# Performance work log

Measured on AMD Instinct MI355X. Metric: run time of the kernel, lower is better.

Reference implementation:

```python
import jax, jax.numpy as jnp
import numpy as np

N_NODES = 50000
N_EDGES = 1600000
IN_SIZE = 128
HIDDEN = 128
OUT_SIZE = 64
NUM_LAYERS = 3
BN_EPS = 1e-5
GIN_EPS_INIT = 1e-5


def setup_inputs() -> dict:
    key = jax.random.key(0)
    ks = jax.random.split(key, 16)
    node_feat = jax.random.normal(ks[0], (N_NODES, IN_SIZE), dtype=jnp.float32)
    src = jax.random.randint(ks[1], (N_EDGES,), 0, N_NODES)
    dst = jax.random.randint(ks[2], (N_EDGES,), 0, N_NODES)
    # per-layer MLP params (in_size == hidden, so shapes are uniform across layers)
    s1 = 1.0 / np.sqrt(IN_SIZE)
    s2 = 1.0 / np.sqrt(HIDDEN)
    W1 = jax.random.uniform(ks[3], (NUM_LAYERS, IN_SIZE, HIDDEN), jnp.float32, -s1, s1)
    b1 = jax.random.uniform(ks[4], (NUM_LAYERS, HIDDEN), jnp.float32, -s1, s1)
    gamma = jnp.ones((NUM_LAYERS, HIDDEN), jnp.float32)
    beta = jnp.zeros((NUM_LAYERS, HIDDEN), jnp.float32)
    W2 = jax.random.uniform(ks[5], (NUM_LAYERS, HIDDEN, HIDDEN), jnp.float32, -s2, s2)
    b2 = jax.random.uniform(ks[6], (NUM_LAYERS, HIDDEN), jnp.float32, -s2, s2)
    eps = jnp.full((NUM_LAYERS,), GIN_EPS_INIT, jnp.float32)  # learnable GIN eps
    Wout = jax.random.uniform(ks[7], (HIDDEN, OUT_SIZE), jnp.float32, -s2, s2)
    bout = jax.random.uniform(ks[8], (OUT_SIZE,), jnp.float32, -s2, s2)
    return {"node_feat": node_feat, "src": src, "dst": dst,
            "W1": W1, "b1": b1, "gamma": gamma, "beta": beta,
            "W2": W2, "b2": b2, "eps": eps, "Wout": Wout, "bout": bout}


def reference(node_feat, src, dst, W1, b1, gamma, beta, W2, b2, eps, Wout, bout):
    n = node_feat.shape[0]
    h = node_feat
    for i in range(NUM_LAYERS):
        # sum-aggregate source features onto destination nodes
        agg = jax.ops.segment_sum(h[src], dst, num_segments=n)  # [N, d]
        x = (1.0 + eps[i]) * h + agg
        x = x @ W1[i] + b1[i]
        # BatchNorm1d (training mode: batch statistics, biased variance)
        mu = jnp.mean(x, axis=0)
        var = jnp.var(x, axis=0)
        x = (x - mu) * jax.lax.rsqrt(var + BN_EPS) * gamma[i] + beta[i]
        x = jax.nn.relu(x)
        h = jax.nn.relu(x @ W2[i] + b2[i])
    return h @ Wout + bout
```

## Files before the change

kernel.cpp:

```cpp
#include <hip/hip_runtime.h>

#define NN 50000
#define NE 1600000
#define HID 128
#define NB 196
#define BCAP 12288

typedef _Float16 half8 __attribute__((ext_vector_type(8)));
typedef float floatx4 __attribute__((ext_vector_type(4)));


__global__ __launch_bounds__(256) void kb_count(const int* __restrict__ dst,
                                                int* __restrict__ gcnt, int E) {
  __shared__ int cnt[NB];
  int tid = threadIdx.x;
  for (int i = tid; i < NB; i += 256) cnt[i] = 0;
  __syncthreads();
  int base = blockIdx.x * 4096;
  for (int i = 0; i < 16; ++i) {
    int e = base + i * 256 + tid;
    if (e < E) atomicAdd(&cnt[dst[e] >> 8], 1);
  }
  __syncthreads();
  for (int i = tid; i < NB; i += 256)
    if (cnt[i]) atomicAdd(&gcnt[i], cnt[i]);
}

__global__ __launch_bounds__(256) void kb_basescan(const int* __restrict__ gcnt,
                                                   int* __restrict__ bbase,
                                                   int* __restrict__ bcur) {
  __shared__ int s[256];
  int tid = threadIdx.x;
  int v = (tid < NB) ? gcnt[tid] : 0;
  s[tid] = v;
  __syncthreads();
  for (int d = 1; d < 256; d <<= 1) {
    int t = (tid >= d) ? s[tid - d] : 0;
    __syncthreads();
    s[tid] += t;
    __syncthreads();
  }
  int incl = s[tid];
  if (tid < NB) {
    bbase[tid] = incl - v;
    bcur[tid] = incl - v;
  }
  if (tid == NB - 1) bbase[NB] = incl;
}

__global__ __launch_bounds__(256) void kb_partition(const int* __restrict__ src,
                                                    const int* __restrict__ dst,
                                                    int* __restrict__ bcur,
                                                    int2* __restrict__ ebuf, int E) {
  __shared__ int cnt[NB];
  __shared__ int sbase[NB];
  int tid = threadIdx.x;
  for (int i = tid; i < NB; i += 256) cnt[i] = 0;
  __syncthreads();
  int base = blockIdx.x * 4096;
  int myd[16], mys[16];
#pragma unroll
  for (int i = 0; i < 16; ++i) {
    int e = base + i * 256 + tid;
    if (e < E) {
      myd[i] = dst[e];
      mys[i] = src[e];
      atomicAdd(&cnt[myd[i] >> 8], 1);
    } else {
      myd[i] = -1;
    }
  }
  __syncthreads();
  for (int i = tid; i < NB; i += 256)
    sbase[i] = cnt[i] ? atomicAdd(&bcur[i], cnt[i]) : 0;
  __syncthreads();
  for (int i = tid; i < NB; i += 256) cnt[i] = 0;
  __syncthreads();
#pragma unroll
  for (int i = 0; i < 16; ++i) {
    if (myd[i] >= 0) {
      int b = myd[i] >> 8;
      int r = atomicAdd(&cnt[b], 1);
      ebuf[sbase[b] + r] = make_int2(mys[i], myd[i]);
    }
  }
}

__global__ __launch_bounds__(256) void kb_csr(const int2* __restrict__ ebuf,
                                              const int* __restrict__ bbase,
                                              int* __restrict__ rs,
                                              int* __restrict__ eidx, int M) {
  __shared__ int cnt[256];
  __shared__ int off[256];
  __shared__ int sbuf[BCAP];
  int tid = threadIdx.x;
  int b = blockIdx.x;
  int lo = bbase[b], hi = bbase[b + 1];
  int n = hi - lo;
  cnt[tid] = 0;
  __syncthreads();
  for (int i = tid; i < n; i += 256) atomicAdd(&cnt[ebuf[lo + i].y & 255], 1);
  __syncthreads();
  int v = cnt[tid];
  off[tid] = v;
  __syncthreads();
  for (int d = 1; d < 256; d <<= 1) {
    int t = (tid >= d) ? off[tid - d] : 0;
    __syncthreads();
    off[tid] += t;
    __syncthreads();
  }
  int excl = off[tid] - v;
  int gnode = b * 256 + tid;
  if (gnode < M) rs[gnode] = lo + excl;
  if (b == NB - 1 && tid == 0) rs[M] = bbase[NB];
  __syncthreads();
  cnt[tid] = excl;
  __syncthreads();
  if (n <= BCAP) {
    for (int i = tid; i < n; i += 256) {
      int2 ed = ebuf[lo + i];
      int r = atomicAdd(&cnt[ed.y & 255], 1);
      sbuf[r] = ed.x;
    }
    __syncthreads();
    for (int i = tid; i < n; i += 256) eidx[lo + i] = sbuf[i];
  } else {
    for (int i = tid; i < n; i += 256) {
      int2 ed = ebuf[lo + i];
      int r = atomicAdd(&cnt[ed.y & 255], 1);
      eidx[lo + r] = ed.x;
    }
  }
}


__global__ __launch_bounds__(256) void k_cvt(const float* __restrict__ x,
                                             _Float16* __restrict__ y, int n8) {
  int t = blockIdx.x * 256 + threadIdx.x;
  if (t >= n8) return;
  const float4* x4 = (const float4*)x;
  float4 u = x4[t * 2], v = x4[t * 2 + 1];
  half8 o;
  o[0] = (_Float16)u.x; o[1] = (_Float16)u.y; o[2] = (_Float16)u.z; o[3] = (_Float16)u.w;
  o[4] = (_Float16)v.x; o[5] = (_Float16)v.y; o[6] = (_Float16)v.z; o[7] = (_Float16)v.w;
  ((half8*)y)[t] = o;
}


__global__ __launch_bounds__(256) void k_pack(const float* __restrict__ W1,
                                              const float* __restrict__ W2,
                                              const float* __restrict__ Wout,
                                              _Float16* __restrict__ wp) {
  int y = blockIdx.y;
  const float* W;
  _Float16* dst;
  int NCT;
  if (y < 3) { W = W1 + (size_t)y * 16384; dst = wp + y * 16384; NCT = 8; }
  else if (y < 6) { W = W2 + (size_t)(y - 3) * 16384; dst = wp + 49152 + (y - 3) * 16384; NCT = 8; }
  else { W = Wout; dst = wp + 98304; NCT = 4; }
  int t = blockIdx.x * 256 + threadIdx.x;
  if (t >= 4 * NCT * 64) return;
  int lane = t & 63;
  int ct = (t >> 6) % NCT;
  int kb = t / (64 * NCT);
  int n = ct * 16 + (lane & 15);
  int k0 = kb * 32 + (lane >> 4) * 8;
  int N = NCT * 16;
#pragma unroll
  for (int j = 0; j < 8; ++j) dst[t * 8 + j] = (_Float16)W[(k0 + j) * N + n];
}


__global__ __launch_bounds__(1024, 8) void k_aggemm1(
    const int* __restrict__ rs, const int* __restrict__ eidx,
    const float* __restrict__ eps, int layer, const _Float16* __restrict__ h,
    const _Float16* __restrict__ wp1, const float* __restrict__ b1L,
    float* __restrict__ csum, float* __restrict__ csq,
    _Float16* __restrict__ x) {
  __shared__ _Float16 As[64 * 136];
  __shared__ float sredS[512];
  __shared__ float sredQ[512];
  const int tid = threadIdx.x;
  const int wid = tid >> 6;
  const int lane = tid & 63;
  const int slot = lane >> 4;
  const int c8 = lane & 15;
  const int rowBase = blockIdx.x * 64;
  const float ep = 1.0f + eps[layer];
  const half8* h8 = (const half8*)h;

  for (int i = 0; i < 4; ++i) {
    const int node = rowBase + wid * 4 + i;
    float a0[8] = {0, 0, 0, 0, 0, 0, 0, 0};
    float a1[8] = {0, 0, 0, 0, 0, 0, 0, 0};
    float a2[8] = {0, 0, 0, 0, 0, 0, 0, 0};
    float a3[8] = {0, 0, 0, 0, 0, 0, 0, 0};
    int e0 = 0, e1 = 0;
    if (node < NN) {
      e0 = rs[node];
      e1 = rs[node + 1];
    }
    int e = e0 + slot;
    for (; e + 12 < e1; e += 16) {
      int s0 = eidx[e];
      int s1 = eidx[e + 4];
      int s2 = eidx[e + 8];
      int s3 = eidx[e + 12];
      half8 v0 = h8[s0 * 16 + c8];
      half8 v1 = h8[s1 * 16 + c8];
      half8 v2 = h8[s2 * 16 + c8];
      half8 v3 = h8[s3 * 16 + c8];
#pragma unroll
      for (int j = 0; j < 8; ++j) {
        a0[j] += (float)v0[j];
        a1[j] += (float)v1[j];
        a2[j] += (float)v2[j];
        a3[j] += (float)v3[j];
      }
    }
    for (; e < e1; e += 4) {
      half8 v = h8[eidx[e] * 16 + c8];
#pragma unroll
      for (int j = 0; j < 8; ++j) a0[j] += (float)v[j];
    }
#pragma unroll
    for (int j = 0; j < 8; ++j) {
      a0[j] += a1[j] + a2[j] + a3[j];
      a0[j] += __shfl_xor(a0[j], 16);
      a0[j] += __shfl_xor(a0[j], 32);
    }
    if (slot == 0) {
      half8 o = {0, 0, 0, 0, 0, 0, 0, 0};
      if (node < NN) {
        half8 hv = h8[node * 16 + c8];
#pragma unroll
        for (int j = 0; j < 8; ++j) o[j] = (_Float16)fmaf(ep, (float)hv[j], a0[j]);
      }
      *(half8*)(As + (wid * 4 + i) * 136 + c8 * 8) = o;
    }
  }
  __syncthreads();

  const int rg = wid & 3;
  const int cg = wid >> 2;
  floatx4 acc[2];
  acc[0] = (floatx4){0.f, 0.f, 0.f, 0.f};
  acc[1] = (floatx4){0.f, 0.f, 0.f, 0.f};
  const half8* wp8 = (const half8*)wp1;
#pragma unroll
  for (int kb = 0; kb < 4; ++kb) {
    half8 a = *(const half8*)(As + (rg * 16 + c8) * 136 + kb * 32 + slot * 8);
#pragma unroll
    for (int t = 0; t < 2; ++t) {
      int ct = cg * 2 + t;
      acc[t] = __builtin_amdgcn_mfma_f32_16x16x32_f16(a, wp8[(kb * 8 + ct) * 64 + lane],
                                                      acc[t], 0, 0, 0);
    }
  }
#pragma unroll
  for (int t = 0; t < 2; ++t) {
    int ct = cg * 2 + t;
    float bv = b1L[ct * 16 + c8];
    float ps = 0.f, pq = 0.f;
#pragma unroll
    for (int reg = 0; reg < 4; ++reg) {
      int row = rg * 16 + slot * 4 + reg;
      int gr = rowBase + row;
      float xv = acc[t][reg] + bv;
      if (gr < NN) {
        x[(size_t)gr * 128 + ct * 16 + c8] = (_Float16)xv;
        ps += xv;
        pq += xv * xv;
      }
    }
    ps += __shfl_xor(ps, 16);
    ps += __shfl_xor(ps, 32);
    pq += __shfl_xor(pq, 16);
    pq += __shfl_xor(pq, 32);
    if (lane < 16) {
      sredS[wid * 32 + t * 16 + lane] = ps;
      sredQ[wid * 32 + t * 16 + lane] = pq;
    }
  }
  __syncthreads();
  if (tid < 128) {
    int c = tid;
    int wbase = (c >> 5) * 4;
    int loc = c & 31;
    float s = sredS[wbase * 32 + loc] + sredS[(wbase + 1) * 32 + loc] +
              sredS[(wbase + 2) * 32 + loc] + sredS[(wbase + 3) * 32 + loc];
    atomicAdd(&csum[c], s);
  } else if (tid < 256) {
    int c = tid - 128;
    int wbase = (c >> 5) * 4;
    int loc = c & 31;
    float q = sredQ[wbase * 32 + loc] + sredQ[(wbase + 1) * 32 + loc] +
              sredQ[(wbase + 2) * 32 + loc] + sredQ[(wbase + 3) * 32 + loc];
    atomicAdd(&csq[c], q);
  }
}


template <int FINAL>
__global__ __launch_bounds__(1024, 8) void k_bn_gemm2(
    const _Float16* __restrict__ x, const _Float16* __restrict__ wp2,
    const float* __restrict__ b2L, const float* __restrict__ gammaL,
    const float* __restrict__ betaL, const float* __restrict__ csum,
    const float* __restrict__ csq, _Float16* __restrict__ hout,
    const _Float16* __restrict__ wpo, const float* __restrict__ boutp,
    float* __restrict__ out) {
  __shared__ _Float16 As[64 * 136];
  const int tid = threadIdx.x;
  const int wid = tid >> 6;
  const int lane = tid & 63;
  const int slot = lane >> 4;
  const int c8 = lane & 15;
  const int c8t = tid & 15;
  const int rowBase = blockIdx.x * 64;

  float sc[8], sh[8];
  {
    const float invM = 1.0f / (float)NN;
#pragma unroll
    for (int j = 0; j < 8; ++j) {
      int k = c8t * 8 + j;
      float mu = csum[k] * invM;
      float var = csq[k] * invM - mu * mu;
      float g = gammaL[k] * rsqrtf(var + 1e-5f);
      sc[j] = g;
      sh[j] = fmaf(-mu, g, betaL[k]);
    }
  }
  {
    int row = tid >> 4;
    int gr = rowBase + row;
    half8 v = {0, 0, 0, 0, 0, 0, 0, 0};
    if (gr < NN) {
      v = *(const half8*)(x + (size_t)gr * 128 + c8t * 8);
#pragma unroll
      for (int j = 0; j < 8; ++j)
        v[j] = (_Float16)fmaxf(fmaf((float)v[j], sc[j], sh[j]), 0.f);
    }
    *(half8*)(As + row * 136 + c8t * 8) = v;
  }
  __syncthreads();

  const int rg = wid & 3;
  const int cg = wid >> 2;
  floatx4 acc[2];
  acc[0] = (floatx4){0.f, 0.f, 0.f, 0.f};
  acc[1] = (floatx4){0.f, 0.f, 0.f, 0.f};
  const half8* wp8 = (const half8*)wp2;
#pragma unroll
  for (int kb = 0; kb < 4; ++kb) {
    half8 a = *(const half8*)(As + (rg * 16 + c8) * 136 + kb * 32 + slot * 8);
#pragma unroll
    for (int t = 0; t < 2; ++t) {
      int ct = cg * 2 + t;
      acc[t] = __builtin_amdgcn_mfma_f32_16x16x32_f16(a, wp8[(kb * 8 + ct) * 64 + lane],
                                                      acc[t], 0, 0, 0);
    }
  }
  __syncthreads();
#pragma unroll
  for (int t = 0; t < 2; ++t) {
    int ct = cg * 2 + t;
    float bv = b2L[ct * 16 + c8];
#pragma unroll
    for (int reg = 0; reg < 4; ++reg) {
      int row = rg * 16 + slot * 4 + reg;
      As[row * 136 + ct * 16 + c8] = (_Float16)fmaxf(acc[t][reg] + bv, 0.f);
    }
  }
  __syncthreads();

  if (FINAL == 0) {
    int row = tid >> 4;
    int gr = rowBase + row;
    if (gr < NN) {
      half8 v = *(half8*)(As + row * 136 + c8t * 8);
      *(half8*)(hout + (size_t)gr * 128 + c8t * 8) = v;
    }
  } else {
    if (cg < 2) {
      floatx4 acc3[2];
      acc3[0] = (floatx4){0.f, 0.f, 0.f, 0.f};
      acc3[1] = (floatx4){0.f, 0.f, 0.f, 0.f};
      const half8* wo8 = (const half8*)wpo;
#pragma unroll
      for (int kb = 0; kb < 4; ++kb) {
        half8 a = *(const half8*)(As + (rg * 16 + c8) * 136 + kb * 32 + slot * 8);
#pragma unroll
        for (int t = 0; t < 2; ++t) {
          int ct = cg * 2 + t;
          acc3[t] = __builtin_amdgcn_mfma_f32_16x16x32_f16(
              a, wo8[(kb * 4 + ct) * 64 + lane], acc3[t], 0, 0, 0);
        }
      }
#pragma unroll
      for (int t = 0; t < 2; ++t) {
        int ct = cg * 2 + t;
        float bv = boutp[ct * 16 + c8];
#pragma unroll
        for (int reg = 0; reg < 4; ++reg) {
          int gr = rowBase + rg * 16 + slot * 4 + reg;
          if (gr < NN) out[(size_t)gr * 64 + ct * 16 + c8] = acc3[t][reg] + bv;
        }
      }
    }
  }
}


extern "C" void kernel_launch(void* const* d_in, const int* in_sizes, int n_in,
                              void* d_out, int out_size, void* d_ws, size_t ws_size,
                              hipStream_t stream) {
  const float* node_feat = (const float*)d_in[0];
  const int* src = (const int*)d_in[1];
  const int* dst = (const int*)d_in[2];
  const float* W1 = (const float*)d_in[3];
  const float* b1 = (const float*)d_in[4];
  const float* gamma = (const float*)d_in[5];
  const float* beta = (const float*)d_in[6];
  const float* W2 = (const float*)d_in[7];
  const float* b2 = (const float*)d_in[8];
  const float* eps = (const float*)d_in[9];
  const float* Wout = (const float*)d_in[10];
  const float* bout = (const float*)d_in[11];
  float* out = (float*)d_out;

  int* rs = (int*)d_ws;
  int* gcnt = rs + 50176;
  int* bbase = gcnt + 256;
  int* bcur = bbase + 256;
  float* stats = (float*)(bcur + 256);
  int* eidx = (int*)(stats + 768);
  _Float16* hb = (_Float16*)(eidx + NE);
  _Float16* xb = hb + (size_t)NN * HID;
  _Float16* wp = xb + (size_t)NN * HID;
  int2* ebuf = (int2*)(wp + 106496);

  hipMemsetAsync(gcnt, 0, (256 * 3 + 768) * sizeof(int), stream);

  k_cvt<<<(NN * HID / 8 + 255) / 256, 256, 0, stream>>>(node_feat, hb, NN * HID / 8);
  k_pack<<<dim3(8, 7), 256, 0, stream>>>(W1, W2, Wout, wp);

  const int partGrid = (NE + 4095) / 4096;
  kb_count<<<partGrid, 256, 0, stream>>>(dst, gcnt, NE);
  kb_basescan<<<1, 256, 0, stream>>>(gcnt, bbase, bcur);
  kb_partition<<<partGrid, 256, 0, stream>>>(src, dst, bcur, ebuf, NE);
  kb_csr<<<NB, 256, 0, stream>>>(ebuf, bbase, rs, eidx, NN);

  const int rowTiles = (NN + 63) / 64;

  for (int L = 0; L < 3; ++L) {
    float* csum = stats + L * 256;
    float* csq = csum + 128;
    k_aggemm1<<<rowTiles, 1024, 0, stream>>>(
        rs, eidx, eps, L, hb, wp + (size_t)L * 16384, b1 + (size_t)L * HID,
        csum, csq, xb);
    if (L < 2) {
      k_bn_gemm2<0><<<rowTiles, 1024, 0, stream>>>(
          xb, wp + 49152 + (size_t)L * 16384, b2 + (size_t)L * HID,
          gamma + (size_t)L * HID, beta + (size_t)L * HID, csum, csq, hb,
          nullptr, nullptr, nullptr);
    } else {
      k_bn_gemm2<1><<<rowTiles, 1024, 0, stream>>>(
          xb, wp + 49152 + (size_t)L * 16384, b2 + (size_t)L * HID,
          gamma + (size_t)L * HID, beta + (size_t)L * HID, csum, csq, nullptr,
          wp + 98304, bout, out);
    }
  }
}
```

Measured before the change: 450.7 us.

## Use persistent blocks with atomic tile counter for aggregate and GEMM kernels

Both the aggregation+GEMM1 kernel and the BN+GEMM2 kernel now launch a fixed grid of 512 persistent 1024-thread blocks. Each block repeatedly grabs 64-row tiles from a global atomic counter, and one counter per launch is zeroed by the existing memset. This is meant to even out load imbalance from irregular node degrees and to amortize per-block setup such as BN scale/shift. The aggregation kernel also stages its GEMM1 output in shared memory so it can write coalesced half8 rows. The cost is extra barriers and an atomic per tile, and the larger per-block count may limit occupancy.

```diff
diff --git a/kernel.cpp b/kernel.cpp
--- a/kernel.cpp
+++ b/kernel.cpp
@@ -5,6 +5,8 @@
 #define HID 128
 #define NB 196
 #define BCAP 12288
+#define NTILES 782
+#define PBLK 512
 
 typedef _Float16 half8 __attribute__((ext_vector_type(8)));
 typedef float floatx4 __attribute__((ext_vector_type(4)));
@@ -177,127 +179,146 @@
     const float* __restrict__ eps, int layer, const _Float16* __restrict__ h,
     const _Float16* __restrict__ wp1, const float* __restrict__ b1L,
     float* __restrict__ csum, float* __restrict__ csq,
-    _Float16* __restrict__ x) {
+    _Float16* __restrict__ x, int* __restrict__ tctr) {
   __shared__ _Float16 As[64 * 136];
   __shared__ float sredS[512];
   __shared__ float sredQ[512];
+  __shared__ int stile;
   const int tid = threadIdx.x;
   const int wid = tid >> 6;
   const int lane = tid & 63;
   const int slot = lane >> 4;
   const int c8 = lane & 15;
-  const int rowBase = blockIdx.x * 64;
+  const int c8t = tid & 15;
   const float ep = 1.0f + eps[layer];
   const half8* h8 = (const half8*)h;
-
-  for (int i = 0; i < 4; ++i) {
-    const int node = rowBase + wid * 4 + i;
-    float a0[8] = {0, 0, 0, 0, 0, 0, 0, 0};
-    float a1[8] = {0, 0, 0, 0, 0, 0, 0, 0};
-    float a2[8] = {0, 0, 0, 0, 0, 0, 0, 0};
-    float a3[8] = {0, 0, 0, 0, 0, 0, 0, 0};
-    int e0 = 0, e1 = 0;
-    if (node < NN) {
-      e0 = rs[node];
-      e1 = rs[node + 1];
-    }
-    int e = e0 + slot;
-    for (; e + 12 < e1; e += 16) {
-      int s0 = eidx[e];
-      int s1 = eidx[e + 4];
-      int s2 = eidx[e + 8];
-      int s3 = eidx[e + 12];
-      half8 v0 = h8[s0 * 16 + c8];
-      half8 v1 = h8[s1 * 16 + c8];
-      half8 v2 = h8[s2 * 16 + c8];
-      half8 v3 = h8[s3 * 16 + c8];
-#pragma unroll
-      for (int j = 0; j < 8; ++j) {
-        a0[j] += (float)v0[j];
-        a1[j] += (float)v1[j];
-        a2[j] += (float)v2[j];
-        a3[j] += (float)v3[j];
-      }
-    }
-    for (; e < e1; e += 4) {
-      half8 v = h8[eidx[e] * 16 + c8];
-#pragma unroll
-      for (int j = 0; j < 8; ++j) a0[j] += (float)v[j];
-    }
-#pragma unroll
-    for (int j = 0; j < 8; ++j) {
-      a0[j] += a1[j] + a2[j] + a3[j];
-      a0[j] += __shfl_xor(a0[j], 16);
-      a0[j] += __shfl_xor(a0[j], 32);
-    }
-    if (slot == 0) {
-      half8 o = {0, 0, 0, 0, 0, 0, 0, 0};
-      if (node < NN) {
-        half8 hv = h8[node * 16 + c8];
-#pragma unroll
-        for (int j = 0; j < 8; ++j) o[j] = (_Float16)fmaf(ep, (float)hv[j], a0[j]);
-      }
-      *(half8*)(As + (wid * 4 + i) * 136 + c8 * 8) = o;
-    }
-  }
-  __syncthreads();
-
+  const half8* wp8 = (const half8*)wp1;
   const int rg = wid & 3;
   const int cg = wid >> 2;
-  floatx4 acc[2];
-  acc[0] = (floatx4){0.f, 0.f, 0.f, 0.f};
-  acc[1] = (floatx4){0.f, 0.f, 0.f, 0.f};
-  const half8* wp8 = (const half8*)wp1;
-#pragma unroll
-  for (int kb = 0; kb < 4; ++kb) {
-    half8 a = *(const half8*)(As + (rg * 16 + c8) * 136 + kb * 32 + slot * 8);
+
+  while (true) {
+    if (tid == 0) stile = atomicAdd(tctr, 1);
+    __syncthreads();
+    const int tile = stile;
+    if (tile >= NTILES) break;
+    const int rowBase = tile * 64;
+
+    for (int i = 0; i < 4; ++i) {
+      const int node = rowBase + wid * 4 + i;
+      float a0[8] = {0, 0, 0, 0, 0, 0, 0, 0};
+      float a1[8] = {0, 0, 0, 0, 0, 0, 0, 0};
+      float a2[8] = {0, 0, 0, 0, 0, 0, 0, 0};
+      float a3[8] = {0, 0, 0, 0, 0, 0, 0, 0};
+      int e0 = 0, e1 = 0;
+      if (node < NN) {
+        e0 = rs[node];
+        e1 = rs[node + 1];
+      }
+      int e = e0 + slot;
+      for (; e + 12 < e1; e += 16) {
+        int s0 = eidx[e];
+        int s1 = eidx[e + 4];
+        int s2 = eidx[e + 8];
+        int s3 = eidx[e + 12];
+        half8 v0 = h8[s0 * 16 + c8];
+        half8 v1 = h8[s1 * 16 + c8];
+        half8 v2 = h8[s2 * 16 + c8];
+        half8 v3 = h8[s3 * 16 + c8];
+#pragma unroll
+        for (int j = 0; j < 8; ++j) {
+          a0[j] += (float)v0[j];
+          a1[j] += (float)v1[j];
+          a2[j] += (float)v2[j];
+          a3[j] += (float)v3[j];
+        }
+      }
+      for (; e < e1; e += 4) {
+        half8 v = h8[eidx[e] * 16 + c8];
+#pragma unroll
+        for (int j = 0; j < 8; ++j) a0[j] += (float)v[j];
+      }
+#pragma unroll
+      for (int j = 0; j < 8; ++j) {
+        a0[j] += a1[j] + a2[j] + a3[j];
+        a0[j] += __shfl_xor(a0[j], 16);
+        a0[j] += __shfl_xor(a0[j], 32);
+      }
+      if (slot == 0) {
+        half8 o = {0, 0, 0, 0, 0, 0, 0, 0};
+        if (node < NN) {
+          half8 hv = h8[node * 16 + c8];
+#pragma unroll
+          for (int j = 0; j < 8; ++j) o[j] = (_Float16)fmaf(ep, (float)hv[j], a0[j]);
+        }
+        *(half8*)(As + (wid * 4 + i) * 136 + c8 * 8) = o;
+      }
+    }
+    __syncthreads();
+
+    floatx4 acc[2];
+    acc[0] = (floatx4){0.f, 0.f, 0.f, 0.f};
+    acc[1] = (floatx4){0.f, 0.f, 0.f, 0.f};
+#pragma unroll
+    for (int kb = 0; kb < 4; ++kb) {
+      half8 a = *(const half8*)(As + (rg * 16 + c8) * 136 + kb * 32 + slot * 8);
+#pragma unroll
+      for (int t = 0; t < 2; ++t) {
+        int ct = cg * 2 + t;
+        acc[t] = __builtin_amdgcn_mfma_f32_16x16x32_f16(
+            a, wp8[(kb * 8 + ct) * 64 + lane], acc[t], 0, 0, 0);
+      }
+    }
+    __syncthreads();
+
 #pragma unroll
     for (int t = 0; t < 2; ++t) {
       int ct = cg * 2 + t;
-      acc[t] = __builtin_amdgcn_mfma_f32_16x16x32_f16(a, wp8[(kb * 8 + ct) * 64 + lane],
-                                                      acc[t], 0, 0, 0);
-    }
-  }
-#pragma unroll
-  for (int t = 0; t < 2; ++t) {
-    int ct = cg * 2 + t;
-    float bv = b1L[ct * 16 + c8];
-    float ps = 0.f, pq = 0.f;
-#pragma unroll
-    for (int reg = 0; reg < 4; ++reg) {
-      int row = rg * 16 + slot * 4 + reg;
+      float bv = b1L[ct * 16 + c8];
+      float ps = 0.f, pq = 0.f;
+#pragma unroll
+      for (int reg = 0; reg < 4; ++reg) {
+        int row = rg * 16 + slot * 4 + reg;
+        float xv = acc[t][reg] + bv;
+        As[row * 136 + ct * 16 + c8] = (_Float16)xv;
+        if (rowBase + row < NN) {
+          ps += xv;
+          pq += xv * xv;
+        }
+      }
+      ps += __shfl_xor(ps, 16);
+      ps += __shfl_xor(ps, 32);
+      pq += __shfl_xor(pq, 16);
+      pq += __shfl_xor(pq, 32);
+      if (lane < 16) {
+        sredS[wid * 32 + t * 16 + lane] = ps;
+        sredQ[wid * 32 + t * 16 + lane] = pq;
+      }
+    }
+    __syncthreads();
+
+    {
+      int row = tid >> 4;
       int gr = rowBase + row;
-      float xv = acc[t][reg] + bv;
       if (gr < NN) {
-        x[(size_t)gr * 128 + ct * 16 + c8] = (_Float16)xv;
-        ps += xv;
-        pq += xv * xv;
-      }
-    }
-    ps += __shfl_xor(ps, 16);
-    ps += __shfl_xor(ps, 32);
-    pq += __shfl_xor(pq, 16);
-    pq += __shfl_xor(pq, 32);
-    if (lane < 16) {
-      sredS[wid * 32 + t * 16 + lane] = ps;
-      sredQ[wid * 32 + t * 16 + lane] = pq;
-    }
-  }
-  __syncthreads();
-  if (tid < 128) {
-    int c = tid;
-    int wbase = (c >> 5) * 4;
-    int loc = c & 31;
-    float s = sredS[wbase * 32 + loc] + sredS[(wbase + 1) * 32 + loc] +
-              sredS[(wbase + 2) * 32 + loc] + sredS[(wbase + 3) * 32 + loc];
-    atomicAdd(&csum[c], s);
-  } else if (tid < 256) {
-    int c = tid - 128;
-    int wbase = (c >> 5) * 4;
-    int loc = c & 31;
-    float q = sredQ[wbase * 32 + loc] + sredQ[(wbase + 1) * 32 + loc] +
-              sredQ[(wbase + 2) * 32 + loc] + sredQ[(wbase + 3) * 32 + loc];
-    atomicAdd(&csq[c], q);
+        half8 v = *(half8*)(As + row * 136 + c8t * 8);
+        *(half8*)(x + (size_t)gr * 128 + c8t * 8) = v;
+      }
+    }
+    if (tid < 128) {
+      int c = tid;
+      int wbase = (c >> 5) * 4;
+      int loc = c & 31;
+      float s = sredS[wbase * 32 + loc] + sredS[(wbase + 1) * 32 + loc] +
+                sredS[(wbase + 2) * 32 + loc] + sredS[(wbase + 3) * 32 + loc];
+      atomicAdd(&csum[c], s);
+    } else if (tid < 256) {
+      int c = tid - 128;
+      int wbase = (c >> 5) * 4;
+      int loc = c & 31;
+      float q = sredQ[wbase * 32 + loc] + sredQ[(wbase + 1) * 32 + loc] +
+                sredQ[(wbase + 2) * 32 + loc] + sredQ[(wbase + 3) * 32 + loc];
+      atomicAdd(&csq[c], q);
+    }
   }
 }
 
@@ -309,15 +330,17 @@
     const float* __restrict__ betaL, const float* __restrict__ csum,
     const float* __restrict__ csq, _Float16* __restrict__ hout,
     const _Float16* __restrict__ wpo, const float* __restrict__ boutp,
-    float* __restrict__ out) {
+    float* __restrict__ out, int* __restrict__ tctr) {
   __shared__ _Float16 As[64 * 136];
+  __shared__ int stile;
   const int tid = threadIdx.x;
   const int wid = tid >> 6;
   const int lane = tid & 63;
   const int slot = lane >> 4;
   const int c8 = lane & 15;
   const int c8t = tid & 15;
-  const int rowBase = blockIdx.x * 64;
+  const int rg = wid & 3;
+  const int cg = wid >> 2;
 
   float sc[8], sh[8];
   {
@@ -332,82 +355,90 @@
       sh[j] = fmaf(-mu, g, betaL[k]);
     }
   }
-  {
-    int row = tid >> 4;
-    int gr = rowBase + row;
-    half8 v = {0, 0, 0, 0, 0, 0, 0, 0};
-    if (gr < NN) {
-      v = *(const half8*)(x + (size_t)gr * 128 + c8t * 8);
-#pragma unroll
-      for (int j = 0; j < 8; ++j)
-        v[j] = (_Float16)fmaxf(fmaf((float)v[j], sc[j], sh[j]), 0.f);
-    }
-    *(half8*)(As + row * 136 + c8t * 8) = v;
-  }
-  __syncthreads();
-
-  const int rg = wid & 3;
-  const int cg = wid >> 2;
-  floatx4 acc[2];
-  acc[0] = (floatx4){0.f, 0.f, 0.f, 0.f};
-  acc[1] = (floatx4){0.f, 0.f, 0.f, 0.f};
-  const half8* wp8 = (const half8*)wp2;
-#pragma unroll
-  for (int kb = 0; kb < 4; ++kb) {
-    half8 a = *(const half8*)(As + (rg * 16 + c8) * 136 + kb * 32 + slot * 8);
+
+  while (true) {
+    if (tid == 0) stile = atomicAdd(tctr, 1);
+    __syncthreads();
+    const int tile = stile;
+    if (tile >= NTILES) break;
+    const int rowBase = tile * 64;
+
+    {
+      int row = tid >> 4;
+      int gr = rowBase + row;
+      half8 v = {0, 0, 0, 0, 0, 0, 0, 0};
+      if (gr < NN) {
+        v = *(const half8*)(x + (size_t)gr * 128 + c8t * 8);
+#pragma unroll
+        for (int j = 0; j < 8; ++j)
+          v[j] = (_Float16)fmaxf(fmaf((float)v[j], sc[j], sh[j]), 0.f);
+      }
+      *(half8*)(As + row * 136 + c8t * 8) = v;
+    }
+    __syncthreads();
+
+    floatx4 acc[2];
+    acc[0] = (floatx4){0.f, 0.f, 0.f, 0.f};
+    acc[1] = (floatx4){0.f, 0.f, 0.f, 0.f};
+    const half8* wp8 = (const half8*)wp2;
+#pragma unroll
+    for (int kb = 0; kb < 4; ++kb) {
+      half8 a = *(const half8*)(As + (rg * 16 + c8) * 136 + kb * 32 + slot * 8);
+#pragma unroll
+      for (int t = 0; t < 2; ++t) {
+        int ct = cg * 2 + t;
+        acc[t] = __builtin_amdgcn_mfma_f32_16x16x32_f16(
+            a, wp8[(kb * 8 + ct) * 64 + lane], acc[t], 0, 0, 0);
+      }
+    }
+    __syncthreads();
 #pragma unroll
     for (int t = 0; t < 2; ++t) {
       int ct = cg * 2 + t;
-      acc[t] = __builtin_amdgcn_mfma_f32_16x16x32_f16(a, wp8[(kb * 8 + ct) * 64 + lane],
-                                                      acc[t], 0, 0, 0);
-    }
-  }
-  __syncthreads();
-#pragma unroll
-  for (int t = 0; t < 2; ++t) {
-    int ct = cg * 2 + t;
-    float bv = b2L[ct * 16 + c8];
-#pragma unroll
-    for (int reg = 0; reg < 4; ++reg) {
-      int row = rg * 16 + slot * 4 + reg;
-      As[row * 136 + ct * 16 + c8] = (_Float16)fmaxf(acc[t][reg] + bv, 0.f);
-    }
-  }
-  __syncthreads();
-
-  if (FINAL == 0) {
-    int row = tid >> 4;
-    int gr = rowBase + row;
-    if (gr < NN) {
-      half8 v = *(half8*)(As + row * 136 + c8t * 8);
-      *(half8*)(hout + (size_t)gr * 128 + c8t * 8) = v;
-    }
-  } else {
-    if (cg < 2) {
-      floatx4 acc3[2];
-      acc3[0] = (floatx4){0.f, 0.f, 0.f, 0.f};
-      acc3[1] = (floatx4){0.f, 0.f, 0.f, 0.f};
-      const half8* wo8 = (const half8*)wpo;
-#pragma unroll
-      for (int kb = 0; kb < 4; ++kb) {
-        half8 a = *(const half8*)(As + (rg * 16 + c8) * 136 + kb * 32 + slot * 8);
+      float bv = b2L[ct * 16 + c8];
+#pragma unroll
+      for (int reg = 0; reg < 4; ++reg) {
+        int row = rg * 16 + slot * 4 + reg;
+        As[row * 136 + ct * 16 + c8] = (_Float16)fmaxf(acc[t][reg] + bv, 0.f);
+      }
+    }
+    __syncthreads();
+
+    if (FINAL == 0) {
+      int row = tid >> 4;
+      int gr = rowBase + row;
+      if (gr < NN) {
+        half8 v = *(half8*)(As + row * 136 + c8t * 8);
+        *(half8*)(hout + (size_t)gr * 128 + c8t * 8) = v;
+      }
+    } else {
+      if (cg < 2) {
+        floatx4 acc3[2];
+        acc3[0] = (floatx4){0.f, 0.f, 0.f, 0.f};
+        acc3[1] = (floatx4){0.f, 0.f, 0.f, 0.f};
+        const half8* wo8 = (const half8*)wpo;
+#pragma unroll
+        for (int kb = 0; kb < 4; ++kb) {
+          half8 a = *(const half8*)(As + (rg * 16 + c8) * 136 + kb * 32 + slot * 8);
+#pragma unroll
+          for (int t = 0; t < 2; ++t) {
+            int ct = cg * 2 + t;
+            acc3[t] = __builtin_amdgcn_mfma_f32_16x16x32_f16(
+                a, wo8[(kb * 4 + ct) * 64 + lane], acc3[t], 0, 0, 0);
+          }
+        }
 #pragma unroll
         for (int t = 0; t < 2; ++t) {
           int ct = cg * 2 + t;
-          acc3[t] = __builtin_amdgcn_mfma_f32_16x16x32_f16(
-              a, wo8[(kb * 4 + ct) * 64 + lane], acc3[t], 0, 0, 0);
+          float bv = boutp[ct * 16 + c8];
+#pragma unroll
+          for (int reg = 0; reg < 4; ++reg) {
+            int gr = rowBase + rg * 16 + slot * 4 + reg;
+            if (gr < NN) out[(size_t)gr * 64 + ct * 16 + c8] = acc3[t][reg] + bv;
+          }
         }
       }
-#pragma unroll
-      for (int t = 0; t < 2; ++t) {
-        int ct = cg * 2 + t;
-        float bv = boutp[ct * 16 + c8];
-#pragma unroll
-        for (int reg = 0; reg < 4; ++reg) {
-          int gr = rowBase + rg * 16 + slot * 4 + reg;
-          if (gr < NN) out[(size_t)gr * 64 + ct * 16 + c8] = acc3[t][reg] + bv;
-        }
-      }
+      __syncthreads();
     }
   }
 }
@@ -435,13 +466,14 @@
   int* bbase = gcnt + 256;
   int* bcur = bbase + 256;
   float* stats = (float*)(bcur + 256);
-  int* eidx = (int*)(stats + 768);
+  int* tctr = (int*)(stats + 768);
+  int* eidx = tctr + 8;
   _Float16* hb = (_Float16*)(eidx + NE);
   _Float16* xb = hb + (size_t)NN * HID;
   _Float16* wp = xb + (size_t)NN * HID;
   int2* ebuf = (int2*)(wp + 106496);
 
-  hipMemsetAsync(gcnt, 0, (256 * 3 + 768) * sizeof(int), stream);
+  hipMemsetAsync(gcnt, 0, (256 * 3 + 768 + 8) * sizeof(int), stream);
 
   k_cvt<<<(NN * HID / 8 + 255) / 256, 256, 0, stream>>>(node_feat, hb, NN * HID / 8);
   k_pack<<<dim3(8, 7), 256, 0, stream>>>(W1, W2, Wout, wp);
@@ -452,24 +484,22 @@
   kb_partition<<<partGrid, 256, 0, stream>>>(src, dst, bcur, ebuf, NE);
   kb_csr<<<NB, 256, 0, stream>>>(ebuf, bbase, rs, eidx, NN);
 
-  const int rowTiles = (NN + 63) / 64;
-
   for (int L = 0; L < 3; ++L) {
     float* csum = stats + L * 256;
     float* csq = csum + 128;
-    k_aggemm1<<<rowTiles, 1024, 0, stream>>>(
+    k_aggemm1<<<PBLK, 1024, 0, stream>>>(
         rs, eidx, eps, L, hb, wp + (size_t)L * 16384, b1 + (size_t)L * HID,
-        csum, csq, xb);
+        csum, csq, xb, tctr + L);
     if (L < 2) {
-      k_bn_gemm2<0><<<rowTiles, 1024, 0, stream>>>(
+      k_bn_gemm2<0><<<PBLK, 1024, 0, stream>>>(
           xb, wp + 49152 + (size_t)L * 16384, b2 + (size_t)L * HID,
           gamma + (size_t)L * HID, beta + (size_t)L * HID, csum, csq, hb,
-          nullptr, nullptr, nullptr);
+          nullptr, nullptr, nullptr, tctr + 3 + L);
     } else {
-      k_bn_gemm2<1><<<rowTiles, 1024, 0, stream>>>(
+      k_bn_gemm2<1><<<PBLK, 1024, 0, stream>>>(
           xb, wp + 49152 + (size_t)L * 16384, b2 + (size_t)L * HID,
           gamma + (size_t)L * HID, beta + (size_t)L * HID, csum, csq, nullptr,
-          wp + 98304, bout, out);
-    }
-  }
-}
+          wp + 98304, bout, out, tctr + 3 + L);
+    }
+  }
+}
```

Measured after the change: 582.3 us. 1.29x slower.
